# Optimization experiments

Measured on AMD Instinct MI355X. Metric: run time of the kernel, lower is better.

Reference implementation:

```python
import jax, jax.numpy as jnp
import numpy as np

C, H, R, INTER = 1024, 16, 16, 2816  # hidden, heads, lora rank, mlp intermediate
B, N = 2, 2048
EPS = 1e-5


def setup_inputs() -> dict:
    key = jax.random.key(0)
    ks = iter(jax.random.split(key, 48))
    w = lambda shape: jax.random.normal(next(ks), shape, jnp.float32) * 0.02
    d = {}
    d["x"] = jax.random.normal(next(ks), (B, N, C), jnp.float32)
    d["y"] = jax.random.normal(next(ks), (B, N, C), jnp.float32)
    d["c"] = jax.random.normal(next(ks), (B, C), jnp.float32)
    # LayerNorms
    d["gx_w"] = jnp.ones((C,)); d["gx_b"] = jnp.zeros((C,))
    d["gy_w"] = jnp.ones((C,)); d["gy_b"] = jnp.zeros((C,))
    # adaLN: SiLU -> Linear(C, 6C)
    d["ada_w"] = w((C, 6 * C)); d["ada_b"] = jnp.zeros((6 * C,))
    # two DoRA cross-attentions
    for p in ("xy", "yx"):
        d[p + "_qkv"] = w((C, 3 * C))
        d[p + "_mag"] = jnp.ones((1, H, 1, 1))
        d[p + "_la"] = w((C, R))
        d[p + "_lb"] = w((R, C))
        d[p + "_proj"] = w((C, C))
    # two HGRN recurrent attentions
    for p in ("ax", "ay"):
        d[p + "_wi"] = w((C, C))
        d[p + "_wf"] = w((C, C))
        d[p + "_wg"] = w((C, C))
        d[p + "_wo"] = w((C, C))
        d[p + "_gn"] = jnp.ones((C,))
    # two gated MLPs
    for p in ("mx", "my"):
        d[p + "_gate"] = w((C, 2 * INTER))
        d[p + "_down"] = w((INTER, C))
    return d


def _ln(v, wgt, b):
    m = v.mean(-1, keepdims=True)
    var = ((v - m) ** 2).mean(-1, keepdims=True)
    return (v - m) / jnp.sqrt(var + EPS) * wgt + b


def _modulate(v, shift, scale):
    return v * (1.0 + scale[:, None, :]) + shift[:, None, :]


def _dora_attn(q_in, Wqkv, mag, la, lb, Wp):
    # NOTE: source ignores key/value args -> self-attention on query stream
    Bq, Nq, Cq = q_in.shape
    D = Cq // H
    qkv = (q_in @ Wqkv).reshape(Bq, Nq, 3, H, D).transpose(2, 0, 3, 1, 4)
    q, k, v = qkv[0], qkv[1], qkv[2]  # [B,H,N,D]
    delta = (q_in @ la) @ lb  # LoRA delta injected into Q
    q = q + mag * delta.reshape(Bq, Nq, H, D).transpose(0, 2, 1, 3)
    attn = jax.nn.softmax(jnp.einsum('bhnd,bhmd->bhnm', q, k) * (D ** -0.5), axis=-1)
    o = jnp.einsum('bhnm,bhmd->bhnd', attn, v).transpose(0, 2, 1, 3).reshape(Bq, Nq, Cq)
    return o @ Wp


def _hgrn_attn(v, wi, wf, wg, wo, gn):
    Bv, Nv, Cv = v.shape
    D = Cv // H
    f = jax.nn.sigmoid(v @ wf)
    i = jax.nn.silu(v @ wi) * (1.0 - f)
    def step(h, ft_it):
        ft, it = ft_it
        h = ft * h + it
        return h, h
    _, hs = jax.lax.scan(step, jnp.zeros((Bv, Cv), v.dtype),
                         (f.transpose(1, 0, 2), i.transpose(1, 0, 2)))
    h = hs.transpose(1, 0, 2).reshape(Bv, Nv, H, D)
    h = h / jnp.sqrt((h * h).mean(-1, keepdims=True) + EPS)  # per-head RMSNorm
    h = (h * gn.reshape(H, D)).reshape(Bv, Nv, Cv)
    return (h * jax.nn.silu(v @ wg)) @ wo


def _mlp(v, wgate, wdown):
    u = v @ wgate
    gate, val = jnp.split(u, 2, axis=-1)
    return (jax.nn.silu(gate) * val) @ wdown


def reference(x, y, c, gx_w, gx_b, gy_w, gy_b, ada_w, ada_b,
              xy_qkv, xy_mag, xy_la, xy_lb, xy_proj,
              yx_qkv, yx_mag, yx_la, yx_lb, yx_proj,
              ax_wi, ax_wf, ax_wg, ax_wo, ax_gn,
              ay_wi, ay_wf, ay_wg, ay_wo, ay_gn,
              mx_gate, mx_down, my_gate, my_down):
    mods = jax.nn.silu(c) @ ada_w + ada_b
    sh_msa, sc_msa, g_msa, sh_mlp, sc_mlp, g_mlp = jnp.split(mods, 6, axis=1)
    x_norm = _ln(x, gx_w, gx_b)
    y_norm = _ln(y, gy_w, gy_b)
    x = x + g_msa[:, None, :] * _dora_attn(x_norm, xy_qkv, xy_mag, xy_la, xy_lb, xy_proj)
    y = y + g_msa[:, None, :] * _dora_attn(y_norm, yx_qkv, yx_mag, yx_la, yx_lb, yx_proj)
    x = x + g_msa[:, None, :] * _hgrn_attn(_modulate(x_norm, sh_msa, sc_msa), ax_wi, ax_wf, ax_wg, ax_wo, ax_gn)
    y = y + g_msa[:, None, :] * _hgrn_attn(_modulate(y_norm, sh_msa, sc_msa), ay_wi, ay_wf, ay_wg, ay_wo, ay_gn)
    x = x + g_mlp[:, None, :] * _mlp(_modulate(_ln(x, gx_w, gx_b), sh_mlp, sc_mlp), mx_gate, mx_down)
    y = y + g_mlp[:, None, :] * _mlp(_modulate(_ln(y, gy_w, gy_b), sh_mlp, sc_mlp), my_gate, my_down)
    return (x, y)
```

## Files before the change

kernel.cpp:

```cpp
#include <hip/hip_runtime.h>
#include <stdint.h>

#define NTOK 2048
#define CDIM 1024
#define ROWS 4096
#define MODS_STRIDE 6144
#define INTERDIM 2816
#define NCHUNK 32
#define CHLEN (NTOK/NCHUNK)

typedef unsigned short u16;
typedef __bf16 bf16x8 __attribute__((ext_vector_type(8)));
typedef float f32x4 __attribute__((ext_vector_type(4)));
typedef u16 u16x8 __attribute__((ext_vector_type(8)));

__device__ __forceinline__ float b2f(u16 u){
  union { unsigned int i; float f; } v; v.i = ((unsigned int)u) << 16; return v.f;
}
__device__ __forceinline__ u16 f2b(float f){
  union { float f; unsigned int i; } v; v.f = f;
  unsigned int i = v.i;
  unsigned int r = i + 0x7FFFu + ((i >> 16) & 1u);
  return (u16)(r >> 16);
}
__device__ __forceinline__ float sigm(float x){ return 1.f/(1.f+__expf(-x)); }
__device__ __forceinline__ float wredsum(float v){
#pragma unroll
  for (int o=32;o>0;o>>=1) v += __shfl_xor(v,o);
  return v;
}
__device__ __forceinline__ void async16(const void* g, void* l){
  __builtin_amdgcn_global_load_lds(
      (const __attribute__((address_space(1))) unsigned int*)g,
      (__attribute__((address_space(3))) unsigned int*)l, 16, 0, 0);
}

__global__ __launch_bounds__(512) void gemm_bt(
    const u16* __restrict__ Ain, const u16* __restrict__ Bt,
    int M, int N, int K, int epi,
    u16* __restrict__ outB,
    float* __restrict__ dest, const float* __restrict__ gate)
{
  __shared__ u16 smem[2][2][2][8192];

  const int nwg  = gridDim.x * gridDim.y;
  const int orig = blockIdx.y * gridDim.x + blockIdx.x;
  const int qch  = nwg >> 3, rch = nwg & 7;
  const int xcd  = orig & 7, loc = orig >> 3;
  const int swzb = (xcd < rch ? xcd*(qch+1) : rch*(qch+1) + (xcd-rch)*qch) + loc;
  const int m0 = (swzb / gridDim.x) * 256;
  const int n0 = (swzb % gridDim.x) * 256;

  const int kchunk = K / gridDim.z;
  const int kbase  = blockIdx.z * kchunk;
  const int NT = kchunk >> 6;

  const int tid = threadIdx.x;
  const int w = tid >> 6, lane = tid & 63;
  const int quad = lane >> 4, l16 = lane & 15;
  const int wm = w >> 2, wn = w & 3;
  const int sx = (l16 & 7) << 4;

  int soff[2];
#pragma unroll
  for (int j=0;j<2;++j){
    const int row = (w*2 + j)*8 + (lane >> 3);
    soff[j] = row*(K*2) + (((lane & 7) ^ (row & 7)) << 4);
  }

  const char* pA0 = (const char*)(Ain + (size_t)m0*K       + kbase);
  const char* pA1 = (const char*)(Ain + (size_t)(m0+128)*K + kbase);
  const char* pB0 = (const char*)(Bt  + (size_t)n0*K       + kbase);
  const char* pB1 = (const char*)(Bt  + (size_t)(n0+128)*K + kbase);

  auto stage = [&](const char* base, int t, u16* region){
#pragma unroll
    for (int j=0;j<2;++j)
      async16(base + (size_t)t*128 + soff[j], (char*)region + (w*2+j)*1024);
  };

  f32x4 acc[8][4] = {};
  bf16x8 af[4][2];
  bf16x8 bq[4][2];

  stage(pA0, 0, &smem[0][0][0][0]);
  stage(pA1, 0, &smem[0][0][1][0]);
  stage(pB0, 0, &smem[0][1][0][0]);
  stage(pB1, 0, &smem[0][1][1][0]);
  if (NT > 1){
    stage(pA0, 1, &smem[1][0][0][0]);
    asm volatile("s_waitcnt vmcnt(2)" ::: "memory");
  } else {
    asm volatile("s_waitcnt vmcnt(0)" ::: "memory");
  }
  __builtin_amdgcn_s_barrier();

#pragma unroll 1
  for (int t=0; t<NT; ++t){
    const int s  = t & 1;
    const int s1 = s ^ 1;
    const char* Ah = (const char*)&smem[s][0][wm][0];
    const char* Bh = (const char*)&smem[s][1][wn>>1][0];
    const int bb = (wn & 1) * 64;

#pragma unroll
    for (int mf=0; mf<4; ++mf)
#pragma unroll
      for (int ks=0; ks<2; ++ks){
        const int b = ((mf*16 + l16)*128 + ks*64 + quad*16) ^ sx;
        af[mf][ks] = *reinterpret_cast<const bf16x8*>(Ah + b);
      }
#pragma unroll
    for (int nf=0; nf<2; ++nf)
#pragma unroll
      for (int ks=0; ks<2; ++ks){
        const int b = ((bb + nf*16 + l16)*128 + ks*64 + quad*16) ^ sx;
        bq[nf][ks] = *reinterpret_cast<const bf16x8*>(Bh + b);
      }
    if (t+1 < NT) stage(pA1, t+1, &smem[s1][0][1][0]);
    __builtin_amdgcn_sched_barrier(0);
    __builtin_amdgcn_s_barrier();
    asm volatile("s_waitcnt lgkmcnt(0)" ::: "memory");
    __builtin_amdgcn_sched_barrier(0);
    __builtin_amdgcn_s_setprio(1);
#pragma unroll
    for (int mf=0; mf<4; ++mf)
#pragma unroll
      for (int nf=0; nf<2; ++nf)
#pragma unroll
        for (int ks=0; ks<2; ++ks)
          acc[mf][nf] = __builtin_amdgcn_mfma_f32_16x16x32_bf16(af[mf][ks], bq[nf][ks], acc[mf][nf], 0,0,0);
    __builtin_amdgcn_s_setprio(0);
    __builtin_amdgcn_sched_barrier(0);
    __builtin_amdgcn_s_barrier();

#pragma unroll
    for (int nf=0; nf<2; ++nf)
#pragma unroll
      for (int ks=0; ks<2; ++ks){
        const int b = ((bb + (2+nf)*16 + l16)*128 + ks*64 + quad*16) ^ sx;
        bq[2+nf][ks] = *reinterpret_cast<const bf16x8*>(Bh + b);
      }
    if (t+1 < NT) stage(pB0, t+1, &smem[s1][1][0][0]);
    __builtin_amdgcn_sched_barrier(0);
    __builtin_amdgcn_s_barrier();
    asm volatile("s_waitcnt lgkmcnt(0)" ::: "memory");
    __builtin_amdgcn_sched_barrier(0);
    __builtin_amdgcn_s_setprio(1);
#pragma unroll
    for (int mf=0; mf<4; ++mf)
#pragma unroll
      for (int nf=0; nf<2; ++nf)
#pragma unroll
        for (int ks=0; ks<2; ++ks)
          acc[mf][2+nf] = __builtin_amdgcn_mfma_f32_16x16x32_bf16(af[mf][ks], bq[2+nf][ks], acc[mf][2+nf], 0,0,0);
    __builtin_amdgcn_s_setprio(0);
    __builtin_amdgcn_sched_barrier(0);
    __builtin_amdgcn_s_barrier();

#pragma unroll
    for (int mf=0; mf<4; ++mf)
#pragma unroll
      for (int ks=0; ks<2; ++ks){
        const int b = ((64 + mf*16 + l16)*128 + ks*64 + quad*16) ^ sx;
        af[mf][ks] = *reinterpret_cast<const bf16x8*>(Ah + b);
      }
    if (t+1 < NT) stage(pB1, t+1, &smem[s1][1][1][0]);
    __builtin_amdgcn_sched_barrier(0);
    __builtin_amdgcn_s_barrier();
    asm volatile("s_waitcnt lgkmcnt(0)" ::: "memory");
    __builtin_amdgcn_sched_barrier(0);
    __builtin_amdgcn_s_setprio(1);
#pragma unroll
    for (int mf=0; mf<4; ++mf)
#pragma unroll
      for (int nf=0; nf<2; ++nf)
#pragma unroll
        for (int ks=0; ks<2; ++ks)
          acc[4+mf][2+nf] = __builtin_amdgcn_mfma_f32_16x16x32_bf16(af[mf][ks], bq[2+nf][ks], acc[4+mf][2+nf], 0,0,0);
    __builtin_amdgcn_s_setprio(0);
    __builtin_amdgcn_sched_barrier(0);
    __builtin_amdgcn_s_barrier();

    if (t+2 < NT) stage(pA0, t+2, &smem[s][0][0][0]);
    __builtin_amdgcn_sched_barrier(0);
    __builtin_amdgcn_s_barrier();
    __builtin_amdgcn_s_setprio(1);
#pragma unroll
    for (int mf=0; mf<4; ++mf)
#pragma unroll
      for (int nf=0; nf<2; ++nf)
#pragma unroll
        for (int ks=0; ks<2; ++ks)
          acc[4+mf][nf] = __builtin_amdgcn_mfma_f32_16x16x32_bf16(af[mf][ks], bq[nf][ks], acc[4+mf][nf], 0,0,0);
    __builtin_amdgcn_s_setprio(0);
    __builtin_amdgcn_sched_barrier(0);
    if (t+2 < NT) asm volatile("s_waitcnt vmcnt(2)" ::: "memory");
    else          asm volatile("s_waitcnt vmcnt(0)" ::: "memory");
    __builtin_amdgcn_s_barrier();
  }

#pragma unroll
  for (int i=0;i<8;++i){
    const int row = m0 + wm*128 + (i>>2)*64 + (i&3)*16 + quad*4;
#pragma unroll
    for (int j=0;j<4;++j){
      const int col = n0 + wn*64 + j*16 + l16;
#pragma unroll
      for (int r=0;r<4;++r){
        const float v = acc[i][j][r];
        const size_t idx = (size_t)(row + r)*N + col;
        if (epi==1){ outB[idx] = f2b(v); }
        else {
          const int b = (row + r) >> 11;
          atomicAdd(&dest[idx], gate[b*MODS_STRIDE + col] * v);
        }
      }
    }
  }
}

struct TDesc { const float* src; u16* dst; int rows; int cols; int base; int dstride; int doff; };
struct TPack { TDesc d[16]; };

__global__ __launch_bounds__(256) void transpose_all(TPack p, int nmat)
{
  __shared__ float t[32][33];
  const int bid = blockIdx.x;
  int mi = 0;
#pragma unroll 1
  while (mi+1 < nmat && bid >= p.d[mi+1].base) ++mi;
  const TDesc D = p.d[mi];
  const int tid2   = bid - D.base;
  const int tilesx = D.cols >> 5;
  const int r0 = (tid2 / tilesx) * 32;
  const int c0 = (tid2 % tilesx) * 32;
  const int tx = threadIdx.x & 31, ty = threadIdx.x >> 5;
  for (int i=ty;i<32;i+=8)
    t[i][tx] = D.src[(size_t)(r0+i)*D.cols + c0 + tx];
  __syncthreads();
  for (int i=ty;i<32;i+=8)
    D.dst[(size_t)(c0+i)*D.dstride + D.doff + r0 + tx] = f2b(t[tx][i]);
}

__global__ __launch_bounds__(256) void ln_kernel(
    const float* __restrict__ xin,
    const float* __restrict__ w, const float* __restrict__ bias,
    const float* __restrict__ mods, int sh_off, int sc_off,
    u16* __restrict__ out_norm, u16* __restrict__ out_mod,
    float* __restrict__ out_xw)
{
  const int row = blockIdx.x;
  const int b = row >> 11;
  const int t = threadIdx.x;
  float v[4];
#pragma unroll
  for (int e=0;e<4;++e)
    v[e] = xin[(size_t)row*CDIM + t*4+e];
  float s  = v[0]+v[1]+v[2]+v[3];
  float ss = v[0]*v[0]+v[1]*v[1]+v[2]*v[2]+v[3]*v[3];
  s = wredsum(s); ss = wredsum(ss);
  __shared__ float rs[4], rss[4];
  const int wv = t>>6;
  if ((t&63)==0){ rs[wv]=s; rss[wv]=ss; }
  __syncthreads();
  s  = rs[0]+rs[1]+rs[2]+rs[3];
  ss = rss[0]+rss[1]+rss[2]+rss[3];
  const float mean = s * (1.f/1024.f);
  const float var  = ss * (1.f/1024.f) - mean*mean;
  const float rinv = rsqrtf(var + 1e-5f);
#pragma unroll
  for (int e=0;e<4;++e){
    const int c = t*4+e;
    const float nv = (v[e]-mean)*rinv*w[c] + bias[c];
    if (out_norm) out_norm[(size_t)row*CDIM+c] = f2b(nv);
    if (out_mod){
      const float sc = mods[b*MODS_STRIDE + sc_off + c];
      const float sh = mods[b*MODS_STRIDE + sh_off + c];
      out_mod[(size_t)row*CDIM+c] = f2b(nv*(1.f+sc)+sh);
    }
    if (out_xw) out_xw[(size_t)row*CDIM+c] = v[e];
  }
}

__global__ __launch_bounds__(256) void ada_init(
    const float* __restrict__ ab, float* __restrict__ mods)
{
  const int j = blockIdx.x*256 + threadIdx.x;
  const int jj = (j >= MODS_STRIDE) ? j - MODS_STRIDE : j;
  mods[j] = ab[jj];
}

__global__ __launch_bounds__(256) void ada_split(
    const float* __restrict__ cin, const float* __restrict__ aw,
    float* __restrict__ mods)
{
  const int j  = blockIdx.x*256 + threadIdx.x;
  const int k0 = blockIdx.y*64;
  float s0 = 0.f, s1 = 0.f;
  for (int k=k0; k<k0+64; ++k){
    const float wv = aw[(size_t)k*MODS_STRIDE + j];
    const float c0 = cin[k], c1 = cin[CDIM + k];
    s0 = fmaf(c0*sigm(c0), wv, s0);
    s1 = fmaf(c1*sigm(c1), wv, s1);
  }
  atomicAdd(&mods[j], s0);
  atomicAdd(&mods[MODS_STRIDE + j], s1);
}

__global__ __launch_bounds__(256) void lora_a(
    const u16* __restrict__ xn, const float* __restrict__ la, float* __restrict__ tmp)
{
  const int r = blockIdx.x;
  const int t = threadIdx.x;
  const int n = t & 15, slice = t >> 4;
  float s = 0.f;
  for (int kk=0;kk<64;++kk){
    const int k = slice*64 + kk;
    s = fmaf(b2f(xn[(size_t)r*CDIM + k]), la[k*16 + n], s);
  }
  __shared__ float red[256];
  red[t] = s;
  __syncthreads();
  if (t < 16){
    float tot = 0.f;
#pragma unroll
    for (int sl=0;sl<16;++sl) tot += red[sl*16 + t];
    tmp[r*16 + t] = tot;
  }
}

__global__ __launch_bounds__(256) void lora_b(
    const float* __restrict__ tmp, const float* __restrict__ lb, u16* __restrict__ delta)
{
  const unsigned int idx = blockIdx.x*256u + threadIdx.x;
  const unsigned int r = idx >> 10, c = idx & 1023u;
  float s = 0.f;
#pragma unroll
  for (int j=0;j<16;++j)
    s = fmaf(tmp[r*16 + j], lb[j*CDIM + c], s);
  delta[idx] = f2b(s);
}

__global__ __launch_bounds__(256) void attn_mfma(
    const u16* __restrict__ qkv, const u16* __restrict__ delta,
    const float* __restrict__ mag, u16* __restrict__ AH)
{
  __shared__ u16 Kl[64*72];
  __shared__ u16 Vt[64*72];
  __shared__ u16 Pl[4][16*72];
  const int t = threadIdx.x;
  const int w = t>>6, lane = t&63;
  const int l16 = lane&15, quad = lane>>4;
  const int qt = blockIdx.x, h = blockIdx.y, b = blockIdx.z;
  const size_t rowbase = (size_t)b*NTOK;
  const float magh = mag[h];

  bf16x8 qf[2];
  {
    const size_t gr = rowbase + qt*64 + w*16 + l16;
    const u16* qp = qkv   + gr*3072 + h*64;
    const u16* dp = delta + gr*1024 + h*64;
#pragma unroll
    for (int kw=0; kw<2; ++kw){
      const int d0 = kw*32 + quad*8;
      const u16x8 qa = *reinterpret_cast<const u16x8*>(qp + d0);
      const u16x8 da = *reinterpret_cast<const u16x8*>(dp + d0);
#pragma unroll
      for (int j=0;j<8;++j)
        qf[kw][j] = (__bf16)((b2f(qa[j]) + magh*b2f(da[j])) * 0.125f);
    }
  }

  float l_part = 0.f;
  f32x4 oacc[4] = {};

  for (int kb=0; kb<32; ++kb){
    __syncthreads();
#pragma unroll
    for (int it=0; it<2; ++it){
      const int e = it*256 + t;
      const int key = e>>3, dc = (e&7)*8;
      const u16x8 kv = *reinterpret_cast<const u16x8*>(
          qkv + (rowbase + kb*64 + key)*3072 + 1024 + h*64 + dc);
      *reinterpret_cast<u16x8*>(&Kl[key*72 + dc]) = kv;
    }
#pragma unroll
    for (int it=0; it<2; ++it){
      const int d0 = (w*2 + it)*8;
      const u16x8 vv = *reinterpret_cast<const u16x8*>(
          qkv + (rowbase + kb*64 + lane)*3072 + 2048 + h*64 + d0);
#pragma unroll
      for (int j=0;j<8;++j)
        Vt[(d0+j)*72 + lane] = vv[j];
    }
    __syncthreads();

    f32x4 sacc[4] = {};
#pragma unroll
    for (int kw=0; kw<2; ++kw){
#pragma unroll
      for (int mt=0; mt<4; ++mt){
        const bf16x8 af = *reinterpret_cast<const bf16x8*>(
            &Kl[(mt*16 + l16)*72 + kw*32 + quad*8]);
        sacc[mt] = __builtin_amdgcn_mfma_f32_16x16x32_bf16(af, qf[kw], sacc[mt], 0,0,0);
      }
    }

#pragma unroll
    for (int mt=0;mt<4;++mt)
#pragma unroll
      for (int r=0;r<4;++r){
        const float pv = __expf(sacc[mt][r]);
        sacc[mt][r] = pv;
        l_part += pv;
      }

#pragma unroll
    for (int mt=0;mt<4;++mt)
#pragma unroll
      for (int rp=0; rp<2; ++rp){
        const unsigned hi = __float_as_uint(sacc[mt][rp*2+1]);
        const unsigned lo = __float_as_uint(sacc[mt][rp*2]);
        *reinterpret_cast<unsigned*>(&Pl[w][l16*72 + mt*16 + quad*4 + rp*2]) =
            (hi & 0xFFFF0000u) | (lo >> 16);
      }

#pragma unroll
    for (int kw=0; kw<2; ++kw){
      const bf16x8 pa = *reinterpret_cast<const bf16x8*>(
          &Pl[w][l16*72 + kw*32 + quad*8]);
#pragma unroll
      for (int dt=0; dt<4; ++dt){
        const bf16x8 vb = *reinterpret_cast<const bf16x8*>(
            &Vt[(dt*16 + l16)*72 + kw*32 + quad*8]);
        oacc[dt] = __builtin_amdgcn_mfma_f32_16x16x32_bf16(pa, vb, oacc[dt], 0,0,0);
      }
    }
  }

  float l_run = l_part;
  l_run += __shfl_xor(l_run, 16);
  l_run += __shfl_xor(l_run, 32);

  float li4[4];
#pragma unroll
  for (int r=0;r<4;++r) li4[r] = __shfl(l_run, quad*4+r);
#pragma unroll
  for (int r=0;r<4;++r){
    const size_t grow = rowbase + qt*64 + w*16 + quad*4 + r;
#pragma unroll
    for (int dt=0; dt<4; ++dt)
      AH[grow*2048 + h*64 + dt*16 + l16] = f2b(oacc[dt][r] / li4[r]);
  }
}

__global__ __launch_bounds__(256) void scan_p1(
    const u16* __restrict__ FIG, float* __restrict__ cA, float* __restrict__ cH)
{
  const unsigned int idx = blockIdx.x*256u + threadIdx.x;
  const unsigned int c = idx & 1023u, chunk = (idx>>10)&(NCHUNK-1), b = idx>>15;
  float A = 1.f, h = 0.f;
  const size_t base = ((size_t)b*NTOK + chunk*CHLEN) * 3072;
  for (int t=0;t<CHLEN;++t){
    const float F = b2f(FIG[base + (size_t)t*3072 + c]);
    const float I = b2f(FIG[base + (size_t)t*3072 + 1024 + c]);
    const float f = sigm(F);
    const float il = I*sigm(I) * (1.f - f);
    A *= f;
    h = fmaf(f, h, il);
  }
  cA[idx] = A; cH[idx] = h;
}

__global__ __launch_bounds__(256) void scan_p2(
    const float* __restrict__ cA, const float* __restrict__ cH, float* __restrict__ Hinit)
{
  const unsigned int idx = blockIdx.x*256u + threadIdx.x;
  const unsigned int b = idx>>10, c = idx&1023u;
  float h = 0.f;
#pragma unroll
  for (int ch=0;ch<NCHUNK;++ch){
    const unsigned int q = (b*NCHUNK + ch)*1024 + c;
    Hinit[q] = h;
    h = fmaf(cA[q], h, cH[q]);
  }
}

__global__ __launch_bounds__(256) void scan_p3(
    const u16* __restrict__ FIG, const float* __restrict__ Hinit, u16* __restrict__ Hb)
{
  const unsigned int idx = blockIdx.x*256u + threadIdx.x;
  const unsigned int c = idx & 1023u, chunk = (idx>>10)&(NCHUNK-1), b = idx>>15;
  float h = Hinit[idx];
  const size_t base = ((size_t)b*NTOK + chunk*CHLEN) * 3072;
  const size_t obase = ((size_t)b*NTOK + chunk*CHLEN) * CDIM;
  for (int t=0;t<CHLEN;++t){
    const float F = b2f(FIG[base + (size_t)t*3072 + c]);
    const float I = b2f(FIG[base + (size_t)t*3072 + 1024 + c]);
    const float f = sigm(F);
    const float il = I*sigm(I) * (1.f - f);
    h = fmaf(f, h, il);
    Hb[obase + (size_t)t*CDIM + c] = f2b(h);
  }
}

__global__ __launch_bounds__(256) void hgrn_post(
    const u16* __restrict__ Hb, const u16* __restrict__ FIG,
    const float* __restrict__ gn, u16* __restrict__ AH)
{
  const int row = blockIdx.x;
  const int t = threadIdx.x;
  float hv[4]; float ss = 0.f;
#pragma unroll
  for (int e=0;e<4;++e){
    hv[e] = b2f(Hb[(size_t)row*CDIM + t*4 + e]);
    ss = fmaf(hv[e], hv[e], ss);
  }
#pragma unroll
  for (int o=1;o<16;o<<=1) ss += __shfl_xor(ss, o);
  const float rinv = rsqrtf(ss*(1.f/64.f) + 1e-5f);
#pragma unroll
  for (int e=0;e<4;++e){
    const int c = t*4+e;
    const float g = b2f(FIG[(size_t)row*3072 + 2048 + c]);
    AH[(size_t)row*2048 + 1024 + c] = f2b(hv[e]*rinv*gn[c] * g*sigm(g));
  }
}

__global__ __launch_bounds__(256) void act_kernel(
    const u16* __restrict__ U, u16* __restrict__ A)
{
  const unsigned int i = blockIdx.x*256u + threadIdx.x;
  const unsigned int r = i / INTERDIM, j = i % INTERDIM;
  const float g = b2f(U[(size_t)r*(2*INTERDIM) + j]);
  const float v = b2f(U[(size_t)r*(2*INTERDIM) + INTERDIM + j]);
  A[i] = f2b(g*sigm(g)*v);
}

__global__ __launch_bounds__(256) void store_out(
    const float* __restrict__ xw, float* __restrict__ out)
{
  const unsigned int i = blockIdx.x*256u + threadIdx.x;
  out[i] = xw[i];
}

__global__ __launch_bounds__(256) void fill_fail(float* __restrict__ out)
{
  const unsigned int i = blockIdx.x*256u + threadIdx.x;
  out[i] = 1234.5f;
}

static void run_stream(hipStream_t stream,
    const float* Xin, const float* LNW, const float* LNB,
    const float* MAG, const float* LA, const float* LBw, const float* GN,
    float* mods, float* xw, float* outp,
    const u16* WqkvT, const u16* WpwT, const u16* WhgrnT,
    const u16* WgateT, const u16* WdownT,
    u16* x_norm, u16* v_h, u16* qkvb, float* tmp, u16* delta, u16* AH,
    float* cA, float* cH, float* Hinit, u16* U, u16* actb)
{
  u16* FIG    = qkvb;
  u16* Hb     = delta;
  u16* mlp_in = x_norm;

  ln_kernel<<<ROWS,256,0,stream>>>(Xin, LNW, LNB, mods, 0, 1024, x_norm, v_h, xw);

  gemm_bt<<<dim3(12,16),512,0,stream>>>(x_norm, WqkvT, ROWS,3072,1024, 1, qkvb, nullptr, nullptr);
  lora_a<<<ROWS,256,0,stream>>>(x_norm, LA, tmp);
  lora_b<<<ROWS*CDIM/256,256,0,stream>>>(tmp, LBw, delta);
  attn_mfma<<<dim3(32,16,2),256,0,stream>>>(qkvb, delta, MAG, AH);

  gemm_bt<<<dim3(12,16),512,0,stream>>>(v_h, WhgrnT, ROWS,3072,1024, 1, FIG, nullptr, nullptr);
  scan_p1<<<2*NCHUNK*1024/256,256,0,stream>>>(FIG, cA, cH);
  scan_p2<<<8,256,0,stream>>>(cA, cH, Hinit);
  scan_p3<<<2*NCHUNK*1024/256,256,0,stream>>>(FIG, Hinit, Hb);
  hgrn_post<<<ROWS,256,0,stream>>>(Hb, FIG, GN, AH);

  gemm_bt<<<dim3(4,16,4),512,0,stream>>>(AH, WpwT, ROWS,1024,2048, 2, nullptr, xw, mods+2048);

  ln_kernel<<<ROWS,256,0,stream>>>(xw, LNW, LNB, mods, 3072, 4096, nullptr, mlp_in, nullptr);
  gemm_bt<<<dim3(22,16),512,0,stream>>>(mlp_in, WgateT, ROWS,5632,1024, 1, U, nullptr, nullptr);
  act_kernel<<<ROWS*INTERDIM/256,256,0,stream>>>(U, actb);
  gemm_bt<<<dim3(4,16,4),512,0,stream>>>(actb, WdownT, ROWS,1024,2816, 2, nullptr, xw, mods+5120);

  store_out<<<ROWS*CDIM/256,256,0,stream>>>(xw, outp);
}

extern "C" void kernel_launch(void* const* d_in, const int* in_sizes, int n_in,
                              void* d_out, int out_size, void* d_ws, size_t ws_size,
                              hipStream_t stream)
{
  const float* X    = (const float*)d_in[0];
  const float* Y    = (const float*)d_in[1];
  const float* Cc   = (const float*)d_in[2];
  const float* GXW  = (const float*)d_in[3];
  const float* GXB  = (const float*)d_in[4];
  const float* GYW  = (const float*)d_in[5];
  const float* GYB  = (const float*)d_in[6];
  const float* ADAW = (const float*)d_in[7];
  const float* ADAB = (const float*)d_in[8];
  const float* XY_QKV = (const float*)d_in[9];
  const float* XY_MAG = (const float*)d_in[10];
  const float* XY_LA  = (const float*)d_in[11];
  const float* XY_LB  = (const float*)d_in[12];
  const float* XY_PROJ= (const float*)d_in[13];
  const float* YX_QKV = (const float*)d_in[14];
  const float* YX_MAG = (const float*)d_in[15];
  const float* YX_LA  = (const float*)d_in[16];
  const float* YX_LB  = (const float*)d_in[17];
  const float* YX_PROJ= (const float*)d_in[18];
  const float* AX_WI = (const float*)d_in[19];
  const float* AX_WF = (const float*)d_in[20];
  const float* AX_WG = (const float*)d_in[21];
  const float* AX_WO = (const float*)d_in[22];
  const float* AX_GN = (const float*)d_in[23];
  const float* AY_WI = (const float*)d_in[24];
  const float* AY_WF = (const float*)d_in[25];
  const float* AY_WG = (const float*)d_in[26];
  const float* AY_WO = (const float*)d_in[27];
  const float* AY_GN = (const float*)d_in[28];
  const float* MX_GATE = (const float*)d_in[29];
  const float* MX_DOWN = (const float*)d_in[30];
  const float* MY_GATE = (const float*)d_in[31];
  const float* MY_DOWN = (const float*)d_in[32];
  float* OUT = (float*)d_out;

  char* p = (char*)d_ws;
  size_t off = 0;
  auto alloc = [&](size_t bytes)->char*{
    char* r = p + off;
    off = (off + bytes + 255) & ~(size_t)255;
    return r;
  };
  float* mods  = (float*)alloc(2*MODS_STRIDE*sizeof(float));
  float* xw_x  = (float*)alloc((size_t)ROWS*CDIM*sizeof(float));
  float* xw_y  = (float*)alloc((size_t)ROWS*CDIM*sizeof(float));
  u16* WqkvT0  = (u16*)alloc((size_t)3072*1024*2);
  u16* WqkvT1  = (u16*)alloc((size_t)3072*1024*2);
  u16* WpwT0   = (u16*)alloc((size_t)1024*2048*2);
  u16* WpwT1   = (u16*)alloc((size_t)1024*2048*2);
  u16* WhgrnT0 = (u16*)alloc((size_t)3072*1024*2);
  u16* WhgrnT1 = (u16*)alloc((size_t)3072*1024*2);
  u16* WgateT0 = (u16*)alloc((size_t)5632*1024*2);
  u16* WgateT1 = (u16*)alloc((size_t)5632*1024*2);
  u16* WdownT0 = (u16*)alloc((size_t)1024*2816*2);
  u16* WdownT1 = (u16*)alloc((size_t)1024*2816*2);
  u16* x_norm  = (u16*)alloc((size_t)ROWS*CDIM*2);
  u16* v_h     = (u16*)alloc((size_t)ROWS*CDIM*2);
  u16* qkvb    = (u16*)alloc((size_t)ROWS*3072*2);
  float* tmp   = (float*)alloc((size_t)ROWS*16*sizeof(float));
  u16* delta   = (u16*)alloc((size_t)ROWS*CDIM*2);
  u16* AH      = (u16*)alloc((size_t)ROWS*2048*2);
  float* cA    = (float*)alloc((size_t)2*NCHUNK*1024*sizeof(float));
  float* cH    = (float*)alloc((size_t)2*NCHUNK*1024*sizeof(float));
  float* Hinit = (float*)alloc((size_t)2*NCHUNK*1024*sizeof(float));
  u16* U       = (u16*)alloc((size_t)ROWS*5632*2);
  u16* actb    = (u16*)alloc((size_t)ROWS*INTERDIM*2);

  if (off > ws_size){
    fill_fail<<<(2*ROWS*CDIM)/256,256,0,stream>>>(OUT);
    return;
  }

  ada_init<<<2*MODS_STRIDE/256,256,0,stream>>>(ADAB, mods);
  ada_split<<<dim3(MODS_STRIDE/256,16),256,0,stream>>>(Cc, ADAW, mods);

  TPack tp; int base = 0; int ndesc = 0;
  auto add = [&](const float* s, u16* d2, int rows, int cols, int dstride, int doff){
    tp.d[ndesc].src = s; tp.d[ndesc].dst = d2;
    tp.d[ndesc].rows = rows; tp.d[ndesc].cols = cols; tp.d[ndesc].base = base;
    tp.d[ndesc].dstride = dstride; tp.d[ndesc].doff = doff;
    base += (rows>>5)*(cols>>5); ++ndesc;
  };
  add(XY_QKV,  WqkvT0, 1024, 3072, 1024, 0);
  add(XY_PROJ, WpwT0,  1024, 1024, 2048, 0);
  add(AX_WO,   WpwT0,  1024, 1024, 2048, 1024);
  add(AX_WF, WhgrnT0,               1024, 1024, 1024, 0);
  add(AX_WI, WhgrnT0 + 1024*1024,   1024, 1024, 1024, 0);
  add(AX_WG, WhgrnT0 + 2*1024*1024, 1024, 1024, 1024, 0);
  add(MX_GATE, WgateT0, 1024, 5632, 1024, 0);
  add(MX_DOWN, WdownT0, 2816, 1024, 2816, 0);
  add(YX_QKV,  WqkvT1, 1024, 3072, 1024, 0);
  add(YX_PROJ, WpwT1,  1024, 1024, 2048, 0);
  add(AY_WO,   WpwT1,  1024, 1024, 2048, 1024);
  add(AY_WF, WhgrnT1,               1024, 1024, 1024, 0);
  add(AY_WI, WhgrnT1 + 1024*1024,   1024, 1024, 1024, 0);
  add(AY_WG, WhgrnT1 + 2*1024*1024, 1024, 1024, 1024, 0);
  add(MY_GATE, WgateT1, 1024, 5632, 1024, 0);
  add(MY_DOWN, WdownT1, 2816, 1024, 2816, 0);
  transpose_all<<<base,256,0,stream>>>(tp, ndesc);

  run_stream(stream, X, GXW, GXB, XY_MAG, XY_LA, XY_LB, AX_GN,
             mods, xw_x, OUT,
             WqkvT0, WpwT0, WhgrnT0, WgateT0, WdownT0,
             x_norm, v_h, qkvb, tmp, delta, AH,
             cA, cH, Hinit, U, actb);

  run_stream(stream, Y, GYW, GYB, YX_MAG, YX_LA, YX_LB, AY_GN,
             mods, xw_y, OUT + (size_t)ROWS*CDIM,
             WqkvT1, WpwT1, WhgrnT1, WgateT1, WdownT1,
             x_norm, v_h, qkvb, tmp, delta, AH,
             cA, cH, Hinit, U, actb);
}
```

Baseline: 1.324 ms.

## Fold LoRA delta into Q weights and pipeline attention K/V loads with swizzled LDS

The LoRA update la@lb, scaled per head by mag, is added straight into the transposed bf16 Q weight columns before the QKV GEMM. This removes the lora_a and lora_b kernels and the delta read in attention. The attention kernel now uses XOR-swizzled unpadded LDS layouts and register double-buffers the next K/V block's global loads while the current block computes. Folding in bf16 adds rounding error to the Q weights. The fold is recomputed on every call, since the weights are re-transposed each launch.

```diff
diff --git a/kernel.cpp b/kernel.cpp
--- a/kernel.cpp
+++ b/kernel.cpp
@@ -243,6 +243,21 @@
     D.dst[(size_t)(c0+i)*D.dstride + D.doff + r0 + tx] = f2b(t[tx][i]);
 }
 
+__global__ __launch_bounds__(256) void lora_fold(
+    const float* __restrict__ la, const float* __restrict__ lb,
+    const float* __restrict__ mag, u16* __restrict__ WqkvT)
+{
+  const unsigned idx = blockIdx.x*256u + threadIdx.x;
+  const int k = idx & 1023, n = idx >> 10;
+  float s = 0.f;
+#pragma unroll
+  for (int r=0;r<16;++r)
+    s = fmaf(la[k*16+r], lb[r*1024+n], s);
+  const float m = mag[n>>6];
+  const unsigned o = (unsigned)n*1024u + k;
+  WqkvT[o] = f2b(b2f(WqkvT[o]) + m*s);
+}
+
 __global__ __launch_bounds__(256) void ln_kernel(
     const float* __restrict__ xin,
     const float* __restrict__ w, const float* __restrict__ bias,
@@ -308,135 +323,138 @@
   atomicAdd(&mods[MODS_STRIDE + j], s1);
 }
 
-__global__ __launch_bounds__(256) void lora_a(
-    const u16* __restrict__ xn, const float* __restrict__ la, float* __restrict__ tmp)
-{
-  const int r = blockIdx.x;
-  const int t = threadIdx.x;
-  const int n = t & 15, slice = t >> 4;
-  float s = 0.f;
-  for (int kk=0;kk<64;++kk){
-    const int k = slice*64 + kk;
-    s = fmaf(b2f(xn[(size_t)r*CDIM + k]), la[k*16 + n], s);
-  }
-  __shared__ float red[256];
-  red[t] = s;
-  __syncthreads();
-  if (t < 16){
-    float tot = 0.f;
-#pragma unroll
-    for (int sl=0;sl<16;++sl) tot += red[sl*16 + t];
-    tmp[r*16 + t] = tot;
-  }
-}
-
-__global__ __launch_bounds__(256) void lora_b(
-    const float* __restrict__ tmp, const float* __restrict__ lb, u16* __restrict__ delta)
-{
-  const unsigned int idx = blockIdx.x*256u + threadIdx.x;
-  const unsigned int r = idx >> 10, c = idx & 1023u;
-  float s = 0.f;
-#pragma unroll
-  for (int j=0;j<16;++j)
-    s = fmaf(tmp[r*16 + j], lb[j*CDIM + c], s);
-  delta[idx] = f2b(s);
-}
-
 __global__ __launch_bounds__(256) void attn_mfma(
-    const u16* __restrict__ qkv, const u16* __restrict__ delta,
-    const float* __restrict__ mag, u16* __restrict__ AH)
-{
-  __shared__ u16 Kl[64*72];
-  __shared__ u16 Vt[64*72];
-  __shared__ u16 Pl[4][16*72];
+    const u16* __restrict__ qkv, u16* __restrict__ AH)
+{
+  __shared__ u16 Kl[64*64];
+  __shared__ u16 Vt[64*64];
+  __shared__ u16 Pl[4][16*64];
   const int t = threadIdx.x;
   const int w = t>>6, lane = t&63;
   const int l16 = lane&15, quad = lane>>4;
   const int qt = blockIdx.x, h = blockIdx.y, b = blockIdx.z;
   const size_t rowbase = (size_t)b*NTOK;
-  const float magh = mag[h];
 
   bf16x8 qf[2];
   {
     const size_t gr = rowbase + qt*64 + w*16 + l16;
-    const u16* qp = qkv   + gr*3072 + h*64;
-    const u16* dp = delta + gr*1024 + h*64;
+    const u16* qp = qkv + gr*3072 + h*64;
 #pragma unroll
     for (int kw=0; kw<2; ++kw){
-      const int d0 = kw*32 + quad*8;
-      const u16x8 qa = *reinterpret_cast<const u16x8*>(qp + d0);
-      const u16x8 da = *reinterpret_cast<const u16x8*>(dp + d0);
+      const u16x8 qa = *reinterpret_cast<const u16x8*>(qp + kw*32 + quad*8);
 #pragma unroll
       for (int j=0;j<8;++j)
-        qf[kw][j] = (__bf16)((b2f(qa[j]) + magh*b2f(da[j])) * 0.125f);
+        qf[kw][j] = (__bf16)(b2f(qa[j]) * 0.125f);
     }
+  }
+
+  const u16* ksrc[2]; int kwr[2];
+#pragma unroll
+  for (int it=0; it<2; ++it){
+    const int e = it*256 + t;
+    const int key = e>>3, ch = e&7;
+    ksrc[it] = qkv + (rowbase + key)*3072 + 1024 + h*64 + ch*8;
+    kwr[it]  = key*128 + ((ch ^ (key&7)) << 4);
+  }
+  const u16* vsrc[2]; int vwr[2][8];
+#pragma unroll
+  for (int it=0; it<2; ++it){
+    const int d0 = (w*2 + it)*8;
+    vsrc[it] = qkv + (rowbase + lane)*3072 + 2048 + h*64 + d0;
+#pragma unroll
+    for (int j=0;j<8;++j){
+      const int d = d0 + j;
+      vwr[it][j] = d*128 + (((lane>>3) ^ (d&7)) << 4) + (lane&7)*2;
+    }
+  }
+  int ra[4][2], pr[2], pw[4][2];
+#pragma unroll
+  for (int x=0; x<4; ++x)
+#pragma unroll
+    for (int kw=0; kw<2; ++kw)
+      ra[x][kw] = (x*16 + l16)*128 + (((kw*4 + quad) ^ (l16&7)) << 4);
+#pragma unroll
+  for (int kw=0; kw<2; ++kw)
+    pr[kw] = l16*128 + (((kw*4 + quad) ^ (l16&7)) << 4);
+#pragma unroll
+  for (int mt=0; mt<4; ++mt)
+#pragma unroll
+    for (int rp=0; rp<2; ++rp){
+      const int bo = (mt*16 + quad*4 + rp*2)*2;
+      pw[mt][rp] = l16*128 + (((bo>>4) ^ (l16&7)) << 4) + (bo & 15);
+    }
+
+  const size_t KSTRIDE = (size_t)64*3072;
+
+  u16x8 kA[2], vA[2], kB[2], vB[2];
+#pragma unroll
+  for (int it=0; it<2; ++it){
+    kA[it] = *reinterpret_cast<const u16x8*>(ksrc[it]);
+    vA[it] = *reinterpret_cast<const u16x8*>(vsrc[it]);
   }
 
   float l_part = 0.f;
   f32x4 oacc[4] = {};
-
-  for (int kb=0; kb<32; ++kb){
-    __syncthreads();
+  char* const pb = (char*)&Pl[w][0];
+
+  auto step = [&](u16x8 (&kk)[2], u16x8 (&vv)[2], int kbn,
+                  u16x8 (&kn)[2], u16x8 (&vn)[2]){
 #pragma unroll
     for (int it=0; it<2; ++it){
-      const int e = it*256 + t;
-      const int key = e>>3, dc = (e&7)*8;
-      const u16x8 kv = *reinterpret_cast<const u16x8*>(
-          qkv + (rowbase + kb*64 + key)*3072 + 1024 + h*64 + dc);
-      *reinterpret_cast<u16x8*>(&Kl[key*72 + dc]) = kv;
-    }
-#pragma unroll
-    for (int it=0; it<2; ++it){
-      const int d0 = (w*2 + it)*8;
-      const u16x8 vv = *reinterpret_cast<const u16x8*>(
-          qkv + (rowbase + kb*64 + lane)*3072 + 2048 + h*64 + d0);
+      *reinterpret_cast<u16x8*>((char*)Kl + kwr[it]) = kk[it];
 #pragma unroll
       for (int j=0;j<8;++j)
-        Vt[(d0+j)*72 + lane] = vv[j];
+        *reinterpret_cast<u16*>((char*)Vt + vwr[it][j]) = vv[it][j];
     }
     __syncthreads();
-
+    {
+      const size_t off = (size_t)kbn * KSTRIDE;
+#pragma unroll
+      for (int it=0; it<2; ++it){
+        kn[it] = *reinterpret_cast<const u16x8*>(ksrc[it] + off);
+        vn[it] = *reinterpret_cast<const u16x8*>(vsrc[it] + off);
+      }
+    }
     f32x4 sacc[4] = {};
 #pragma unroll
-    for (int kw=0; kw<2; ++kw){
+    for (int kw=0; kw<2; ++kw)
 #pragma unroll
       for (int mt=0; mt<4; ++mt){
-        const bf16x8 af = *reinterpret_cast<const bf16x8*>(
-            &Kl[(mt*16 + l16)*72 + kw*32 + quad*8]);
+        const bf16x8 af = *reinterpret_cast<const bf16x8*>((char*)Kl + ra[mt][kw]);
         sacc[mt] = __builtin_amdgcn_mfma_f32_16x16x32_bf16(af, qf[kw], sacc[mt], 0,0,0);
       }
-    }
-
-#pragma unroll
-    for (int mt=0;mt<4;++mt)
+#pragma unroll
+    for (int mt=0; mt<4; ++mt)
 #pragma unroll
       for (int r=0;r<4;++r){
         const float pv = __expf(sacc[mt][r]);
         sacc[mt][r] = pv;
         l_part += pv;
       }
-
-#pragma unroll
-    for (int mt=0;mt<4;++mt)
+#pragma unroll
+    for (int mt=0; mt<4; ++mt)
 #pragma unroll
       for (int rp=0; rp<2; ++rp){
         const unsigned hi = __float_as_uint(sacc[mt][rp*2+1]);
         const unsigned lo = __float_as_uint(sacc[mt][rp*2]);
-        *reinterpret_cast<unsigned*>(&Pl[w][l16*72 + mt*16 + quad*4 + rp*2]) =
-            (hi & 0xFFFF0000u) | (lo >> 16);
-      }
-
+        *reinterpret_cast<unsigned*>(pb + pw[mt][rp]) = (hi & 0xFFFF0000u) | (lo >> 16);
+      }
 #pragma unroll
     for (int kw=0; kw<2; ++kw){
-      const bf16x8 pa = *reinterpret_cast<const bf16x8*>(
-          &Pl[w][l16*72 + kw*32 + quad*8]);
+      const bf16x8 pa = *reinterpret_cast<const bf16x8*>(pb + pr[kw]);
 #pragma unroll
       for (int dt=0; dt<4; ++dt){
-        const bf16x8 vb = *reinterpret_cast<const bf16x8*>(
-            &Vt[(dt*16 + l16)*72 + kw*32 + quad*8]);
+        const bf16x8 vb = *reinterpret_cast<const bf16x8*>((char*)Vt + ra[dt][kw]);
         oacc[dt] = __builtin_amdgcn_mfma_f32_16x16x32_bf16(pa, vb, oacc[dt], 0,0,0);
       }
     }
+    __syncthreads();
+  };
+
+#pragma unroll 1
+  for (int kb=0; kb<32; kb+=2){
+    step(kA, vA, (kb+1 < 32 ? kb+1 : 31), kB, vB);
+    step(kB, vB, (kb+2 < 32 ? kb+2 : 31), kA, vA);
   }
 
   float l_run = l_part;
@@ -555,21 +573,21 @@
     const float* Xin, const float* LNW, const float* LNB,
     const float* MAG, const float* LA, const float* LBw, const float* GN,
     float* mods, float* xw, float* outp,
-    const u16* WqkvT, const u16* WpwT, const u16* WhgrnT,
+    u16* WqkvT, const u16* WpwT, const u16* WhgrnT,
     const u16* WgateT, const u16* WdownT,
-    u16* x_norm, u16* v_h, u16* qkvb, float* tmp, u16* delta, u16* AH,
+    u16* x_norm, u16* v_h, u16* qkvb, u16* delta, u16* AH,
     float* cA, float* cH, float* Hinit, u16* U, u16* actb)
 {
   u16* FIG    = qkvb;
   u16* Hb     = delta;
   u16* mlp_in = x_norm;
 
+  lora_fold<<<4096,256,0,stream>>>(LA, LBw, MAG, WqkvT);
+
   ln_kernel<<<ROWS,256,0,stream>>>(Xin, LNW, LNB, mods, 0, 1024, x_norm, v_h, xw);
 
   gemm_bt<<<dim3(12,16),512,0,stream>>>(x_norm, WqkvT, ROWS,3072,1024, 1, qkvb, nullptr, nullptr);
-  lora_a<<<ROWS,256,0,stream>>>(x_norm, LA, tmp);
-  lora_b<<<ROWS*CDIM/256,256,0,stream>>>(tmp, LBw, delta);
-  attn_mfma<<<dim3(32,16,2),256,0,stream>>>(qkvb, delta, MAG, AH);
+  attn_mfma<<<dim3(32,16,2),256,0,stream>>>(qkvb, AH);
 
   gemm_bt<<<dim3(12,16),512,0,stream>>>(v_h, WhgrnT, ROWS,3072,1024, 1, FIG, nullptr, nullptr);
   scan_p1<<<2*NCHUNK*1024/256,256,0,stream>>>(FIG, cA, cH);
@@ -649,7 +667,6 @@
   u16* x_norm  = (u16*)alloc((size_t)ROWS*CDIM*2);
   u16* v_h     = (u16*)alloc((size_t)ROWS*CDIM*2);
   u16* qkvb    = (u16*)alloc((size_t)ROWS*3072*2);
-  float* tmp   = (float*)alloc((size_t)ROWS*16*sizeof(float));
   u16* delta   = (u16*)alloc((size_t)ROWS*CDIM*2);
   u16* AH      = (u16*)alloc((size_t)ROWS*2048*2);
   float* cA    = (float*)alloc((size_t)2*NCHUNK*1024*sizeof(float));
@@ -694,12 +711,12 @@
   run_stream(stream, X, GXW, GXB, XY_MAG, XY_LA, XY_LB, AX_GN,
              mods, xw_x, OUT,
              WqkvT0, WpwT0, WhgrnT0, WgateT0, WdownT0,
-             x_norm, v_h, qkvb, tmp, delta, AH,
+             x_norm, v_h, qkvb, delta, AH,
              cA, cH, Hinit, U, actb);
 
   run_stream(stream, Y, GYW, GYB, YX_MAG, YX_LA, YX_LB, AY_GN,
              mods, xw_y, OUT + (size_t)ROWS*CDIM,
              WqkvT1, WpwT1, WhgrnT1, WgateT1, WdownT1,
-             x_norm, v_h, qkvb, tmp, delta, AH,
+             x_norm, v_h, qkvb, delta, AH,
              cA, cH, Hinit, U, actb);
 }
```

Result: faster. 1.262 ms (-4.7%).
